# Optimization experiments

Measured on AMD Instinct MI355X. Metric: run time of the kernel, lower is better.

The kernel has to match this reference:

```python
import jax, jax.numpy as jnp
import numpy as np

N_NODES = 100000
N_EDGES = 300000
D_IN = 256
D_OUT = 256


def setup_inputs() -> dict:
    key = jax.random.key(0)
    k1, k2, k3 = jax.random.split(key, 3)
    z = jax.random.normal(k1, (N_NODES, D_IN), dtype=jnp.float32)
    edge_index = jax.random.randint(k2, (2, N_EDGES), 0, N_NODES, dtype=jnp.int64)
    # Linear(input_dim, out_dim): weight [out, in], stored transposed for x @ W
    W = jax.random.normal(k3, (D_IN, D_OUT), dtype=jnp.float32) / np.sqrt(D_IN)
    b = jnp.zeros((D_OUT,), dtype=jnp.float32)
    return {"z": z, "edge_index": edge_index, "W": W, "b": b}


def reference(z, edge_index, W, b):
    # h = Linear(z): [N, D_out]
    h = z @ W + b
    # gather endpoint embeddings and take per-edge dot product
    src = h[edge_index[0]]  # [E, D_out]
    dst = h[edge_index[1]]  # [E, D_out]
    value = jnp.sum(src * dst, axis=1)  # [E]
    return jax.nn.sigmoid(value)
```

## Files before the change

### kernel.cpp

```cpp
#include <hip/hip_runtime.h>
#include <hip/hip_bf16.h>
#include <hip/hip_fp16.h>
#include <math.h>


#define D_DIM 256

typedef __attribute__((ext_vector_type(8))) _Float16 half8;
typedef __attribute__((ext_vector_type(4))) float f32x4;

__device__ half8 g_Wf[8 * 256 * 4];

__global__ __launch_bounds__(256) void pack_w_kernel(const float* __restrict__ W) {
  int t = blockIdx.x * 256 + threadIdx.x;
  int kb = t >> 10;
  int qd = (t >> 8) & 3;
  int n  = t & 255;
  int fn = n >> 4;
  int fr = n & 15;
  half8 o;
#pragma unroll
  for (int j = 0; j < 8; j++)
    o[j] = (_Float16)W[(size_t)(kb * 32 + qd * 8 + j) * D_DIM + n];
  g_Wf[kb * 1024 + fn * 64 + qd * 16 + fr] = o;
}

__global__ __launch_bounds__(512, 2) void gemm_mfma_kernel(
    const float* __restrict__ z, const float* __restrict__ b,
    __half* __restrict__ h, int nrows) {
  __shared__ char smem[131072 + 8 * 2176];
  const int tid = threadIdx.x;
  const int lane = tid & 63;
  const int wv = tid >> 6;
  const int fr = lane & 15;
  const int qd = lane >> 4;

  {
    const char* gsrc = (const char*)g_Wf;
#pragma unroll
    for (int rnd = 0; rnd < 16; rnd++) {
      int off = rnd * 8192 + wv * 1024;
      __builtin_amdgcn_global_load_lds(
          (const __attribute__((address_space(1))) void*)(gsrc + off + lane * 16),
          (__attribute__((address_space(3))) void*)(smem + off),
          16, 0, 0);
    }
  }
  float bias[16];
#pragma unroll
  for (int fn = 0; fn < 16; fn++) bias[fn] = b[fn * 16 + fr];

  __syncthreads();

  const half8* bw = (const half8*)smem;
  __half* et = (__half*)(smem + 131072 + wv * 2176);

  const int gw = blockIdx.x * 8 + wv;
  const int nstrips = (nrows + 15) >> 4;

#pragma unroll 1
  for (int s = gw; s < nstrips; s += 2048) {
    int r = s * 16 + fr;
    r = r < nrows ? r : (nrows - 1);
    const float* zr = z + (size_t)r * D_DIM + qd * 8;

    float4 a0[8], a1[8];
#pragma unroll
    for (int kb = 0; kb < 8; kb++) {
      a0[kb] = *(const float4*)(zr + kb * 32);
      a1[kb] = *(const float4*)(zr + kb * 32 + 4);
    }
    asm volatile("" ::: "memory");

    f32x4 acc[16];
#pragma unroll
    for (int fn = 0; fn < 16; fn++) acc[fn] = (f32x4)0.f;

#pragma unroll
    for (int kb = 0; kb < 8; kb++) {
      half8 af;
      af[0] = (_Float16)a0[kb].x; af[1] = (_Float16)a0[kb].y;
      af[2] = (_Float16)a0[kb].z; af[3] = (_Float16)a0[kb].w;
      af[4] = (_Float16)a1[kb].x; af[5] = (_Float16)a1[kb].y;
      af[6] = (_Float16)a1[kb].z; af[7] = (_Float16)a1[kb].w;
#pragma unroll
      for (int fn = 0; fn < 16; fn++) {
        half8 bf = bw[kb * 1024 + fn * 64 + lane];
        acc[fn] = __builtin_amdgcn_mfma_f32_16x16x32_f16(af, bf, acc[fn], 0, 0, 0);
      }
    }

#pragma unroll
    for (int ph = 0; ph < 2; ph++) {
#pragma unroll
      for (int ch = 0; ch < 2; ch++) {
        if ((qd >> 1) == ph) {
#pragma unroll
          for (int f2 = 0; f2 < 8; f2++) {
            int fn = ch * 8 + f2;
#pragma unroll
            for (int rr = 0; rr < 4; rr++)
              et[((qd & 1) * 4 + rr) * 136 + f2 * 16 + fr] =
                  __float2half(acc[fn][rr] + bias[fn]);
          }
        }
#pragma unroll
        for (int p = 0; p < 2; p++) {
          int idx = p * 64 + lane;
          int rr = idx >> 4;
          int cc = idx & 15;
          float4 v = *(const float4*)(et + rr * 136 + cc * 8);
          int row = s * 16 + ph * 8 + rr;
          if (row < nrows)
            *(float4*)(h + (size_t)row * D_DIM + ch * 128 + cc * 8) = v;
        }
      }
    }
  }
}

__global__ __launch_bounds__(256) void edge_dot_kernel(
    const int* __restrict__ ei, const __half* __restrict__ h,
    float* __restrict__ out, int E) {
  int wid = (blockIdx.x * blockDim.x + threadIdx.x) >> 6;
  int lane = threadIdx.x & 63;
  int ebase = wid * 8;
  if (ebase >= E) return;
  const int half = lane >> 5;
  const int off = lane & 31;

  float4 v[8];
#pragma unroll
  for (int q = 0; q < 8; q++) {
    int e = ebase + q;
    e = e < E ? e : (E - 1);
    int node = half ? ei[E + e] : ei[e];
    v[q] = *(const float4*)((const __half*)h + (size_t)node * D_DIM + off * 8);
  }

  float res = 0.f;
#pragma unroll
  for (int q = 0; q < 8; q++) {
    float4 w;
    w.x = __shfl_xor(v[q].x, 32);
    w.y = __shfl_xor(v[q].y, 32);
    w.z = __shfl_xor(v[q].z, 32);
    w.w = __shfl_xor(v[q].w, 32);
    const __half2* a2 = (const __half2*)&v[q];
    const __half2* b2 = (const __half2*)&w;
    float part = 0.f;
#pragma unroll
    for (int j = 0; j < 4; j++) {
      float2 fa = __half22float2(a2[j]);
      float2 fb = __half22float2(b2[j]);
      part += fa.x * fb.x + fa.y * fb.y;
    }
#pragma unroll
    for (int m = 1; m <= 16; m <<= 1) part += __shfl_xor(part, m);
    res = (lane == q) ? part : res;
  }
  if (lane < 8) {
    int e = ebase + lane;
    if (e < E) out[e] = 1.0f / (1.0f + __expf(-res));
  }
}

extern "C" void kernel_launch(void* const* d_in, const int* in_sizes, int n_in,
                              void* d_out, int out_size, void* d_ws, size_t ws_size,
                              hipStream_t stream) {
  const float* z  = (const float*)d_in[0];
  const int*   ei = (const int*)d_in[1];
  const float* W  = (const float*)d_in[2];
  const float* b  = (const float*)d_in[3];
  float* out = (float*)d_out;
  __half* h  = (__half*)d_ws;

  const int nnodes = in_sizes[0] / D_DIM;
  const int E = in_sizes[1] / 2;

  pack_w_kernel<<<32, 256, 0, stream>>>(W);

  gemm_mfma_kernel<<<256, 512, 0, stream>>>(z, b, h, nnodes);

  int waves = (E + 7) / 8;
  dim3 grid_edge(((size_t)waves * 64 + 255) / 256);
  edge_dot_kernel<<<grid_edge, 256, 0, stream>>>(ei, h, out, E);
}
```

Before: 215.4 us.

## Fuse W packing into GEMM kernel and software-prefetch next strip of z

Removes the separate pack_w kernel launch. Each GEMM block now reads W directly, converts it to fp16 and writes it into LDS in the MFMA layout. The GEMM loop also prefetches the next strip's z rows into registers while the current strip's MFMAs run, so global load latency overlaps compute. The cost is that all 256 blocks redundantly convert W with scattered 2-byte LDS stores, and register pressure rises from holding both af and the prefetched a0/a1.

```diff
diff --git a/kernel.cpp b/kernel.cpp
--- a/kernel.cpp
+++ b/kernel.cpp
@@ -9,25 +9,9 @@
 typedef __attribute__((ext_vector_type(8))) _Float16 half8;
 typedef __attribute__((ext_vector_type(4))) float f32x4;
 
-__device__ half8 g_Wf[8 * 256 * 4];
-
-__global__ __launch_bounds__(256) void pack_w_kernel(const float* __restrict__ W) {
-  int t = blockIdx.x * 256 + threadIdx.x;
-  int kb = t >> 10;
-  int qd = (t >> 8) & 3;
-  int n  = t & 255;
-  int fn = n >> 4;
-  int fr = n & 15;
-  half8 o;
-#pragma unroll
-  for (int j = 0; j < 8; j++)
-    o[j] = (_Float16)W[(size_t)(kb * 32 + qd * 8 + j) * D_DIM + n];
-  g_Wf[kb * 1024 + fn * 64 + qd * 16 + fr] = o;
-}
-
 __global__ __launch_bounds__(512, 2) void gemm_mfma_kernel(
-    const float* __restrict__ z, const float* __restrict__ b,
-    __half* __restrict__ h, int nrows) {
+    const float* __restrict__ z, const float* __restrict__ W,
+    const float* __restrict__ b, __half* __restrict__ h, int nrows) {
   __shared__ char smem[131072 + 8 * 2176];
   const int tid = threadIdx.x;
   const int lane = tid & 63;
@@ -36,14 +20,21 @@
   const int qd = lane >> 4;
 
   {
-    const char* gsrc = (const char*)g_Wf;
+    __half* lp = (__half*)smem;
+    const float4* W4 = (const float4*)W;
+#pragma unroll 8
+    for (int i = 0; i < 32; i++) {
+      int q = i * 512 + tid;
+      int k = q >> 6;
+      int n0 = (q & 63) * 4;
+      float4 w = W4[q];
+      int kb = k >> 5, kqd = (k >> 3) & 3, j = k & 7;
 #pragma unroll
-    for (int rnd = 0; rnd < 16; rnd++) {
-      int off = rnd * 8192 + wv * 1024;
-      __builtin_amdgcn_global_load_lds(
-          (const __attribute__((address_space(1))) void*)(gsrc + off + lane * 16),
-          (__attribute__((address_space(3))) void*)(smem + off),
-          16, 0, 0);
+      for (int u = 0; u < 4; u++) {
+        int n = n0 + u;
+        int fi = kb * 1024 + (n >> 4) * 64 + kqd * 16 + (n & 15);
+        lp[fi * 8 + j] = __float2half(((const float*)&w)[u]);
+      }
     }
   }
   float bias[16];
@@ -58,37 +49,52 @@
   const int gw = blockIdx.x * 8 + wv;
   const int nstrips = (nrows + 15) >> 4;
 
+  int r0 = gw * 16 + fr;
+  r0 = r0 < nrows ? r0 : (nrows - 1);
+  const float* zr0 = z + (size_t)r0 * D_DIM + qd * 8;
+
+  float4 a0[8], a1[8];
+#pragma unroll
+  for (int kb = 0; kb < 8; kb++) {
+    a0[kb] = *(const float4*)(zr0 + kb * 32);
+    a1[kb] = *(const float4*)(zr0 + kb * 32 + 4);
+  }
+  asm volatile("" ::: "memory");
+
 #pragma unroll 1
   for (int s = gw; s < nstrips; s += 2048) {
-    int r = s * 16 + fr;
-    r = r < nrows ? r : (nrows - 1);
-    const float* zr = z + (size_t)r * D_DIM + qd * 8;
-
-    float4 a0[8], a1[8];
+    half8 af[8];
 #pragma unroll
     for (int kb = 0; kb < 8; kb++) {
-      a0[kb] = *(const float4*)(zr + kb * 32);
-      a1[kb] = *(const float4*)(zr + kb * 32 + 4);
+      af[kb][0] = (_Float16)a0[kb].x; af[kb][1] = (_Float16)a0[kb].y;
+      af[kb][2] = (_Float16)a0[kb].z; af[kb][3] = (_Float16)a0[kb].w;
+      af[kb][4] = (_Float16)a1[kb].x; af[kb][5] = (_Float16)a1[kb].y;
+      af[kb][6] = (_Float16)a1[kb].z; af[kb][7] = (_Float16)a1[kb].w;
+    }
+
+    int snext = s + 2048;
+    if (snext < nstrips) {
+      int rn = snext * 16 + fr;
+      rn = rn < nrows ? rn : (nrows - 1);
+      const float* zrn = z + (size_t)rn * D_DIM + qd * 8;
+#pragma unroll
+      for (int kb = 0; kb < 8; kb++) {
+        a0[kb] = *(const float4*)(zrn + kb * 32);
+        a1[kb] = *(const float4*)(zrn + kb * 32 + 4);
+      }
     }
     asm volatile("" ::: "memory");
 
     f32x4 acc[16];
 #pragma unroll
     for (int fn = 0; fn < 16; fn++) acc[fn] = (f32x4)0.f;
-
 #pragma unroll
-    for (int kb = 0; kb < 8; kb++) {
-      half8 af;
-      af[0] = (_Float16)a0[kb].x; af[1] = (_Float16)a0[kb].y;
-      af[2] = (_Float16)a0[kb].z; af[3] = (_Float16)a0[kb].w;
-      af[4] = (_Float16)a1[kb].x; af[5] = (_Float16)a1[kb].y;
-      af[6] = (_Float16)a1[kb].z; af[7] = (_Float16)a1[kb].w;
+    for (int kb = 0; kb < 8; kb++)
 #pragma unroll
       for (int fn = 0; fn < 16; fn++) {
         half8 bf = bw[kb * 1024 + fn * 64 + lane];
-        acc[fn] = __builtin_amdgcn_mfma_f32_16x16x32_f16(af, bf, acc[fn], 0, 0, 0);
+        acc[fn] = __builtin_amdgcn_mfma_f32_16x16x32_f16(af[kb], bf, acc[fn], 0, 0, 0);
       }
-    }
 
 #pragma unroll
     for (int ph = 0; ph < 2; ph++) {
@@ -178,9 +184,7 @@
   const int nnodes = in_sizes[0] / D_DIM;
   const int E = in_sizes[1] / 2;
 
-  pack_w_kernel<<<32, 256, 0, stream>>>(W);
-
-  gemm_mfma_kernel<<<256, 512, 0, stream>>>(z, b, h, nnodes);
+  gemm_mfma_kernel<<<256, 512, 0, stream>>>(z, W, b, h, nnodes);
 
   int waves = (E + 7) / 8;
   dim3 grid_edge(((size_t)waves * 64 + 255) / 256);
```

New measurement: 227.8 us. 5.8% more time.

## Split GEMM strips across waves by output columns with double-buffered LDS A tiles

Applied to the files above, without the earlier changes.

The GEMM changes from one wave owning a 16-row strip across all 256 output columns to a block-wide 16-row strip in which each wave computes 32 columns. The z tile is converted to fp16 and staged in a swizzled, double-buffered LDS tile, and the next strip's global loads are prefetched while the current one computes. This cuts per-wave register use and the redundant A conversions. In exchange it adds two block barriers per strip and drops the occupancy hint of two blocks per CU. Because only 256 blocks process one strip each per iteration, the latency-hiding parallelism may be lower than before.

```diff
diff --git a/kernel.cpp b/kernel.cpp
--- a/kernel.cpp
+++ b/kernel.cpp
@@ -5,8 +5,10 @@
 
 
 #define D_DIM 256
+#define NBLK 256
 
 typedef __attribute__((ext_vector_type(8))) _Float16 half8;
+typedef __attribute__((ext_vector_type(4))) _Float16 half4;
 typedef __attribute__((ext_vector_type(4))) float f32x4;
 
 __device__ half8 g_Wf[8 * 256 * 4];
@@ -25,10 +27,23 @@
   g_Wf[kb * 1024 + fn * 64 + qd * 16 + fr] = o;
 }
 
-__global__ __launch_bounds__(512, 2) void gemm_mfma_kernel(
+__device__ inline void stage_write(char* tile, int tid, float4 A, float4 B) {
+  int row = tid >> 6;
+  int inner = (tid & 63) * 8;
+  int sw = (row & 7) << 4;
+  half4 p0, p1;
+  p0[0] = (_Float16)A.x; p0[1] = (_Float16)A.y;
+  p0[2] = (_Float16)A.z; p0[3] = (_Float16)A.w;
+  p1[0] = (_Float16)B.x; p1[1] = (_Float16)B.y;
+  p1[2] = (_Float16)B.z; p1[3] = (_Float16)B.w;
+  *(half4*)(tile + row * 512 + (inner ^ sw)) = p0;
+  *(half4*)(tile + (row + 8) * 512 + (inner ^ sw)) = p1;
+}
+
+__global__ __launch_bounds__(512) void gemm_mfma_kernel(
     const float* __restrict__ z, const float* __restrict__ b,
     __half* __restrict__ h, int nrows) {
-  __shared__ char smem[131072 + 8 * 2176];
+  __shared__ char smem[147456];
   const int tid = threadIdx.x;
   const int lane = tid & 63;
   const int wv = tid >> 6;
@@ -46,76 +61,70 @@
           16, 0, 0);
     }
   }
-  float bias[16];
-#pragma unroll
-  for (int fn = 0; fn < 16; fn++) bias[fn] = b[fn * 16 + fr];
+  float bias0 = b[wv * 32 + fr];
+  float bias1 = b[wv * 32 + 16 + fr];
 
+  char* atile0 = smem + 131072;
+  char* atile1 = smem + 139264;
+  const char* zb = (const char*)z;
+  const int nstrips = (nrows + 15) >> 4;
+
+  int s0 = blockIdx.x;
+  float4 ld0, ld1;
+  {
+    const char* sb = zb + (size_t)s0 * 16384;
+    ld0 = *(const float4*)(sb + tid * 16);
+    ld1 = *(const float4*)(sb + 8192 + tid * 16);
+  }
+  stage_write(atile0, tid, ld0, ld1);
   __syncthreads();
 
   const half8* bw = (const half8*)smem;
-  __half* et = (__half*)(smem + 131072 + wv * 2176);
-
-  const int gw = blockIdx.x * 8 + wv;
-  const int nstrips = (nrows + 15) >> 4;
+  int cur = 0;
 
 #pragma unroll 1
-  for (int s = gw; s < nstrips; s += 2048) {
-    int r = s * 16 + fr;
-    r = r < nrows ? r : (nrows - 1);
-    const float* zr = z + (size_t)r * D_DIM + qd * 8;
+  for (int s = s0; s < nstrips; s += NBLK) {
+    char* at = cur ? atile1 : atile0;
+    char* an = cur ? atile0 : atile1;
+    const bool hasnext = (s + NBLK) < nstrips;
 
-    float4 a0[8], a1[8];
-#pragma unroll
-    for (int kb = 0; kb < 8; kb++) {
-      a0[kb] = *(const float4*)(zr + kb * 32);
-      a1[kb] = *(const float4*)(zr + kb * 32 + 4);
+    if (hasnext) {
+      const char* sb = zb + (size_t)(s + NBLK) * 16384;
+      ld0 = *(const float4*)(sb + tid * 16);
+      ld1 = *(const float4*)(sb + 8192 + tid * 16);
     }
     asm volatile("" ::: "memory");
 
-    f32x4 acc[16];
-#pragma unroll
-    for (int fn = 0; fn < 16; fn++) acc[fn] = (f32x4)0.f;
-
+    f32x4 acc0 = (f32x4)0.f, acc1 = (f32x4)0.f;
+    const char* abase = at + fr * 512;
+    const int sw = (fr & 7) << 4;
 #pragma unroll
     for (int kb = 0; kb < 8; kb++) {
-      half8 af;
-      af[0] = (_Float16)a0[kb].x; af[1] = (_Float16)a0[kb].y;
-      af[2] = (_Float16)a0[kb].z; af[3] = (_Float16)a0[kb].w;
-      af[4] = (_Float16)a1[kb].x; af[5] = (_Float16)a1[kb].y;
-      af[6] = (_Float16)a1[kb].z; af[7] = (_Float16)a1[kb].w;
+      half8 af = *(const half8*)(abase + ((kb * 64 + qd * 16) ^ sw));
+      half8 bf0 = bw[kb * 1024 + (2 * wv) * 64 + lane];
+      half8 bf1 = bw[kb * 1024 + (2 * wv + 1) * 64 + lane];
+      acc0 = __builtin_amdgcn_mfma_f32_16x16x32_f16(af, bf0, acc0, 0, 0, 0);
+      acc1 = __builtin_amdgcn_mfma_f32_16x16x32_f16(af, bf1, acc1, 0, 0, 0);
+    }
+    __syncthreads();
+
+    __half* et = (__half*)(at + wv * 1024);
 #pragma unroll
-      for (int fn = 0; fn < 16; fn++) {
-        half8 bf = bw[kb * 1024 + fn * 64 + lane];
-        acc[fn] = __builtin_amdgcn_mfma_f32_16x16x32_f16(af, bf, acc[fn], 0, 0, 0);
-      }
+    for (int r = 0; r < 4; r++) {
+      et[(qd * 4 + r) * 32 + fr]      = __float2half(acc0[r] + bias0);
+      et[(qd * 4 + r) * 32 + 16 + fr] = __float2half(acc1[r] + bias1);
     }
+    int row = lane >> 2, c = lane & 3;
+    float4 v = *(const float4*)((const char*)et + row * 64 + c * 16);
 
-#pragma unroll
-    for (int ph = 0; ph < 2; ph++) {
-#pragma unroll
-      for (int ch = 0; ch < 2; ch++) {
-        if ((qd >> 1) == ph) {
-#pragma unroll
-          for (int f2 = 0; f2 < 8; f2++) {
-            int fn = ch * 8 + f2;
-#pragma unroll
-            for (int rr = 0; rr < 4; rr++)
-              et[((qd & 1) * 4 + rr) * 136 + f2 * 16 + fr] =
-                  __float2half(acc[fn][rr] + bias[fn]);
-          }
-        }
-#pragma unroll
-        for (int p = 0; p < 2; p++) {
-          int idx = p * 64 + lane;
-          int rr = idx >> 4;
-          int cc = idx & 15;
-          float4 v = *(const float4*)(et + rr * 136 + cc * 8);
-          int row = s * 16 + ph * 8 + rr;
-          if (row < nrows)
-            *(float4*)(h + (size_t)row * D_DIM + ch * 128 + cc * 8) = v;
-        }
-      }
-    }
+    if (hasnext) stage_write(an, tid, ld0, ld1);
+
+    int grow = s * 16 + row;
+    if (grow < nrows)
+      *(float4*)((char*)h + (size_t)grow * 512 + wv * 64 + c * 16) = v;
+
+    cur ^= 1;
+    __syncthreads();
   }
 }
 
@@ -180,7 +189,7 @@
 
   pack_w_kernel<<<32, 256, 0, stream>>>(W);
 
-  gemm_mfma_kernel<<<256, 512, 0, stream>>>(z, b, h, nnodes);
+  gemm_mfma_kernel<<<NBLK, 512, 0, stream>>>(z, b, h, nnodes);
 
   int waves = (E + 7) / 8;
   dim3 grid_edge(((size_t)waves * 64 + 255) / 256);
```

After: 202.4 us. -6.0%, faster.
